# Kernel optimization log

Hardware: AMD Instinct MI355X
Metric: run time of the kernel (lower is better)

The kernel has to match this reference:

```python
import jax, jax.numpy as jnp
import numpy as np
from jax import lax

B, C, H, W = 16, 128, 128, 128
K = 3
EPS = 1e-8


def setup_inputs() -> dict:
    key = jax.random.key(0)
    k1, k2, k3 = jax.random.split(key, 3)
    x = jax.random.normal(k1, (B, C, H, W), dtype=jnp.float32)
    style = jax.random.normal(k2, (B, C), dtype=jnp.float32)
    weight = jax.random.normal(k3, (C, C, K, K), dtype=jnp.float32)
    return {"x": x, "style": style, "weight": weight}


def reference(x, style, weight):
    b = x.shape[0]
    o, i, kh, kw = weight.shape
    h, w_sp = x.shape[2], x.shape[3]
    # style / ||style||_inf over channel dim (per-sample scalar)
    s = style / jnp.max(jnp.abs(style), axis=1, keepdims=True)          # (B, i)
    # weight * (1/sqrt(i*kh*kw)) / ||weight||_inf over (i,kh,kw) per out channel
    wmax = jnp.max(jnp.abs(weight), axis=(1, 2, 3), keepdims=True)      # (o,1,1,1)
    wn = weight * (1.0 / jnp.sqrt(jnp.float32(i * kh * kw)) / wmax)     # (o,i,kh,kw)
    # per-sample modulation over input channels
    wmod = wn[None] * s[:, None, :, None, None]                         # (B,o,i,kh,kw)
    # demodulation (coe reshaped to (i,1,1,1) in torch; valid since o==i)
    coe = lax.rsqrt(jnp.sum(jnp.square(wmod), axis=(2, 3, 4)) + EPS)    # (B,o)
    wmod = wmod * coe[:, :, None, None, None]
    # fused batched conv via grouped-conv trick (StyleGAN2-style)
    xr = x.reshape(1, b * i, h, w_sp)
    wr = wmod.reshape(b * o, i, kh, kw)
    out = lax.conv_general_dilated(
        xr, wr,
        window_strides=(1, 1),
        padding=[(1, 1), (1, 1)],
        feature_group_count=b,
        dimension_numbers=("NCHW", "OIHW", "NCHW"),
    )
    return out.reshape(b, o, h, w_sp)
```

## Files before the change

### kernel.cpp

```cpp
#include <hip/hip_runtime.h>
#include <hip/hip_bf16.h>


#define BATCH 16
#define CH    128
#define HW    128
#define WPITCH 1152

#define WS_WMAX 0
#define WS_SN   128
#define WS_AFAC 2176
#define WS_WT   4224
#define WFRAG_BYTE_OFF 606720
#define WFRAG_BYTES    4718592
#define WS_NEEDED      (WFRAG_BYTE_OFF + WFRAG_BYTES)

typedef short  s8v  __attribute__((ext_vector_type(8)));
typedef float  f4v  __attribute__((ext_vector_type(4)));
typedef float  f2v  __attribute__((ext_vector_type(2)));

__device__ inline unsigned short f2bf(float f) {
    union { float f; unsigned int u; } v; v.f = f;
    unsigned int r = v.u + 0x7FFFu + ((v.u >> 16) & 1u);
    return (unsigned short)(r >> 16);
}

__global__ __launch_bounds__(256) void k0_transpose(const float* __restrict__ w,
                                                    float* __restrict__ ws) {
    int idx = blockIdx.x * 256 + threadIdx.x;
    if (idx < CH * WPITCH) {
        int kt = idx >> 7;
        int o  = idx & 127;
        ws[WS_WT + idx] = w[(size_t)o * WPITCH + kt];
    }
}

__global__ __launch_bounds__(256) void k1_norms(const float* __restrict__ style,
                                                const float* __restrict__ weight,
                                                float* __restrict__ ws) {
    __shared__ float red[4];
    const int bid = blockIdx.x;
    const int t = threadIdx.x;
    if (bid < 128) {
        const int o = bid;
        float m = 0.f;
        for (int idx = t; idx < WPITCH; idx += 256)
            m = fmaxf(m, fabsf(weight[(size_t)o * WPITCH + idx]));
        #pragma unroll
        for (int off = 32; off > 0; off >>= 1)
            m = fmaxf(m, __shfl_down(m, off, 64));
        if ((t & 63) == 0) red[t >> 6] = m;
        __syncthreads();
        if (t == 0)
            ws[WS_WMAX + o] = fmaxf(fmaxf(red[0], red[1]), fmaxf(red[2], red[3]));
    } else {
        const int b = bid - 128;
        float v = (t < CH) ? style[b * CH + t] : 0.f;
        float m = fabsf(v);
        #pragma unroll
        for (int off = 32; off > 0; off >>= 1)
            m = fmaxf(m, __shfl_down(m, off, 64));
        if ((t & 63) == 0) red[t >> 6] = m;
        __syncthreads();
        float smax = fmaxf(fmaxf(red[0], red[1]), fmaxf(red[2], red[3]));
        if (t < CH) ws[WS_SN + b * CH + t] = v / smax;
    }
}

__global__ __launch_bounds__(256) void k2_coe(const float* __restrict__ weight,
                                              float* __restrict__ ws) {
    const int o = blockIdx.x;
    const int b = blockIdx.y;
    const int t = threadIdx.x;
    const float* sn = ws + WS_SN + b * CH;
    float s = 0.f;
    for (int idx = t; idx < WPITCH; idx += 256) {
        int i = idx / 9;
        float v = weight[(size_t)o * WPITCH + idx] * sn[i];
        s += v * v;
    }
    #pragma unroll
    for (int off = 32; off > 0; off >>= 1) s += __shfl_down(s, off, 64);
    __shared__ float red[4];
    if ((t & 63) == 0) red[t >> 6] = s;
    __syncthreads();
    if (t == 0) {
        float S = red[0] + red[1] + red[2] + red[3];
        float wm = ws[WS_WMAX + o];
        float scale = 1.0f / (sqrtf(1152.0f) * wm);
        float coe = rsqrtf(scale * scale * S + 1e-8f);
        ws[WS_AFAC + b * CH + o] = scale * coe;
    }
}

__global__ __launch_bounds__(256) void k3_swz(const float* __restrict__ ws,
                                              const float* __restrict__ weight,
                                              unsigned short* __restrict__ wfrag) {
    int t = blockIdx.x * 256 + threadIdx.x;
    const int lane = t & 63;
    int f = t >> 6;
    const int mo = f & 7;  f >>= 3;
    const int ci = f & 3;  f >>= 2;
    const int kk = f % 9;
    const int b  = f / 9;
    const int o  = mo * 16 + (lane & 15);
    const int i0 = ci * 32 + (lane >> 4) * 8;
    const float af = ws[WS_AFAC + b * CH + o];
    union { unsigned short u[8]; uint4 v; } pk;
    #pragma unroll
    for (int j = 0; j < 8; ++j) {
        int i = i0 + j;
        float v = weight[(size_t)o * WPITCH + i * 9 + kk] * af * ws[WS_SN + b * CH + i];
        pk.u[j] = f2bf(v);
    }
    *(uint4*)(wfrag + (size_t)t * 8) = pk.v;
}

#define XROW 132
#define XIP  40

__global__ __launch_bounds__(256, 2) void k4_mfma(const float* __restrict__ x,
                                                  const unsigned short* __restrict__ wfrag,
                                                  float* __restrict__ out) {
    const int h0 = blockIdx.x * 2;
    const int b  = blockIdx.y;
    const int t  = threadIdx.x;
    const int lane = t & 63;
    const int w    = t >> 6;
    const int ohalf = w & 1;
    const int rsel  = w >> 1;
    const int ln15  = lane & 15;
    const int quad  = lane >> 4;

    __shared__ unsigned short xT[4 * XROW * XIP];

    if (t < 32) {
        const int zr   = t & 3;
        const int zibk = (t >> 2) & 3;
        const int zc   = (t >> 4) ? 129 : 0;
        *(s8v*)&xT[(zr * XROW + zc) * XIP + zibk * 8] = (s8v){0, 0, 0, 0, 0, 0, 0, 0};
    }

    f4v acc[4][8];
    #pragma unroll
    for (int mt = 0; mt < 4; ++mt)
        #pragma unroll
        for (int nt = 0; nt < 8; ++nt)
            acc[mt][nt] = (f4v){0.f, 0.f, 0.f, 0.f};

    const int  cp     = t & 63;
    const int  sr     = w;
    const int  srow   = h0 - 1 + sr;
    const bool svalid = (unsigned)srow < 128u;
    const int  srcl   = svalid ? srow : 0;

    #pragma unroll 1
    for (int ci = 0; ci < 4; ++ci) {
        const int ib = ci * 32;
        __syncthreads();

        #pragma unroll
        for (int it = 0; it < 4; ++it) {
            const float* xp = x + (((size_t)(b * CH + ib + it * 8)) * HW + srcl) * HW + 2 * cp;
            f2v d[8];
            #pragma unroll
            for (int j = 0; j < 8; ++j)
                d[j] = *(const f2v*)(xp + (size_t)j * HW * HW);
            union { unsigned short u[16]; s8v v[2]; } pk;
            #pragma unroll
            for (int j = 0; j < 8; ++j) {
                pk.u[j]     = f2bf(svalid ? d[j].x : 0.f);
                pk.u[8 + j] = f2bf(svalid ? d[j].y : 0.f);
            }
            *(s8v*)&xT[(sr * XROW + (2 * cp + 1)) * XIP + it * 8] = pk.v[0];
            *(s8v*)&xT[(sr * XROW + (2 * cp + 2)) * XIP + it * 8] = pk.v[1];
        }
        __syncthreads();

        s8v aN[4];
        #pragma unroll
        for (int mt = 0; mt < 4; ++mt) {
            const int mo = ohalf * 4 + mt;
            aN[mt] = *(const s8v*)(wfrag +
                     ((size_t)(((b * 9 + 0) * 4 + ci) * 8 + mo) * 64 + lane) * 8);
        }
        #pragma unroll 1
        for (int kk = 0; kk < 9; ++kk) {
            s8v aC[4];
            #pragma unroll
            for (int mt = 0; mt < 4; ++mt) aC[mt] = aN[mt];
            const int kn = (kk < 8) ? kk + 1 : 8;
            #pragma unroll
            for (int mt = 0; mt < 4; ++mt) {
                const int mo = ohalf * 4 + mt;
                aN[mt] = *(const s8v*)(wfrag +
                         ((size_t)(((b * 9 + kn) * 4 + ci) * 8 + mo) * 64 + lane) * 8);
            }
            const int ky = kk / 3;
            const int kx = kk - ky * 3;
            const int r  = rsel + ky;
            s8v bf[8];
            #pragma unroll
            for (int nt = 0; nt < 8; ++nt) {
                const int c = nt * 16 + ln15 + kx;
                bf[nt] = *(const s8v*)&xT[(r * XROW + c) * XIP + quad * 8];
            }
            #pragma unroll
            for (int mt = 0; mt < 4; ++mt)
                #pragma unroll
                for (int nt = 0; nt < 8; ++nt)
                    acc[mt][nt] = __builtin_amdgcn_mfma_f32_16x16x32_bf16(
                        aC[mt], bf[nt], acc[mt][nt], 0, 0, 0);
        }
    }

    const int orow = h0 + rsel;
    #pragma unroll
    for (int mt = 0; mt < 4; ++mt) {
        int o = ohalf * 64 + mt * 16 + quad * 4;
        #pragma unroll
        for (int nt = 0; nt < 8; ++nt) {
            int xcol = nt * 16 + ln15;
            float* op = out + (((size_t)(b * CH + o)) * HW + orow) * HW + xcol;
            #pragma unroll
            for (int reg = 0; reg < 4; ++reg)
                op[(size_t)reg * HW * HW] = acc[mt][nt][reg];
        }
    }
}

#define TI    8
#define XPITCH 132
__global__ __launch_bounds__(256) void k3_conv(const float* __restrict__ x,
                                               const float* __restrict__ ws,
                                               float* __restrict__ out) {
    const int h = blockIdx.x;
    const int b = blockIdx.y;
    const int t = threadIdx.x;
    const int og = t >> 4;
    const int pg = t & 15;

    __shared__ float x_lds[TI * 3 * XPITCH];
    __shared__ float w_lds[TI * 9 * 128];
    __shared__ float Af_l[128];
    __shared__ float sn_l[128];

    if (t < 128) {
        Af_l[t] = ws[WS_AFAC + b * CH + t];
        sn_l[t] = ws[WS_SN + b * CH + t];
    }
    float acc[8][8];
    #pragma unroll
    for (int j = 0; j < 8; ++j)
        #pragma unroll
        for (int p = 0; p < 8; ++p) acc[j][p] = 0.f;

    const float4* wt4 = (const float4*)(ws + WS_WT);
    float4* w_lds4 = (float4*)w_lds;
    const float4* Af4 = (const float4*)Af_l;

    #pragma unroll 1
    for (int ci = 0; ci < CH / TI; ++ci) {
        const int ib = ci * TI;
        __syncthreads();
        for (int idx = t; idx < TI * 3 * 130; idx += 256) {
            int ti  = idx / 390;
            int rem = idx - ti * 390;
            int r   = rem / 130;
            int c   = rem - r * 130;
            int row = h + r - 1;
            int col = c - 1;
            float v = 0.f;
            if ((unsigned)row < 128u && (unsigned)col < 128u)
                v = x[(((size_t)b * CH + ib + ti) * HW + row) * HW + col];
            x_lds[(ti * 3 + r) * XPITCH + c] = v;
        }
        for (int idx = t; idx < TI * 9 * 32; idx += 256) {
            int kt = idx >> 5;
            int o4 = idx & 31;
            int ti = kt / 9;
            float4 wv = wt4[(size_t)ib * 9 * 32 + idx];
            float4 af = Af4[o4];
            float  s  = sn_l[ib + ti];
            float4 rr;
            rr.x = wv.x * af.x * s; rr.y = wv.y * af.y * s;
            rr.z = wv.z * af.z * s; rr.w = wv.w * af.w * s;
            w_lds4[idx] = rr;
        }
        __syncthreads();
        #pragma unroll 1
        for (int ti = 0; ti < TI; ++ti) {
            float xv[3][12];
            #pragma unroll
            for (int ky = 0; ky < 3; ++ky)
                #pragma unroll
                for (int q = 0; q < 3; ++q) {
                    float4 v = *(const float4*)&x_lds[(ti * 3 + ky) * XPITCH + pg * 8 + q * 4];
                    xv[ky][q*4+0] = v.x; xv[ky][q*4+1] = v.y;
                    xv[ky][q*4+2] = v.z; xv[ky][q*4+3] = v.w;
                }
            #pragma unroll
            for (int kk = 0; kk < 9; ++kk) {
                const int ky = kk / 3;
                const int kx = kk % 3;
                float wv[8];
                #pragma unroll
                for (int q = 0; q < 2; ++q) {
                    float4 v = *(const float4*)&w_lds[(ti * 9 + kk) * 128 + og * 8 + q * 4];
                    wv[q*4+0] = v.x; wv[q*4+1] = v.y; wv[q*4+2] = v.z; wv[q*4+3] = v.w;
                }
                #pragma unroll
                for (int j = 0; j < 8; ++j)
                    #pragma unroll
                    for (int p = 0; p < 8; ++p)
                        acc[j][p] = fmaf(wv[j], xv[ky][p + kx], acc[j][p]);
            }
        }
    }
    const size_t obase = ((size_t)b * CH) * (HW * HW) + (size_t)h * HW;
    #pragma unroll
    for (int j = 0; j < 8; ++j) {
        int o = og * 8 + j;
        float4 v0 = {acc[j][0], acc[j][1], acc[j][2], acc[j][3]};
        float4 v1 = {acc[j][4], acc[j][5], acc[j][6], acc[j][7]};
        *(float4*)&out[obase + (size_t)o * (HW * HW) + pg * 8]     = v0;
        *(float4*)&out[obase + (size_t)o * (HW * HW) + pg * 8 + 4] = v1;
    }
}

extern "C" void kernel_launch(void* const* d_in, const int* in_sizes, int n_in,
                              void* d_out, int out_size, void* d_ws, size_t ws_size,
                              hipStream_t stream) {
    const float* x      = (const float*)d_in[0];
    const float* style  = (const float*)d_in[1];
    const float* weight = (const float*)d_in[2];
    float* out = (float*)d_out;
    float* ws  = (float*)d_ws;

    k1_norms<<<144, 256, 0, stream>>>(style, weight, ws);
    k2_coe<<<dim3(CH, BATCH), 256, 0, stream>>>(weight, ws);

    if (ws_size >= (size_t)WS_NEEDED) {
        unsigned short* wfrag = (unsigned short*)((char*)d_ws + WFRAG_BYTE_OFF);
        k3_swz<<<1152, 256, 0, stream>>>(ws, weight, wfrag);
        k4_mfma<<<dim3(HW / 2, BATCH), 256, 0, stream>>>(x, wfrag, out);
    } else {
        k0_transpose<<<(CH * WPITCH + 255) / 256, 256, 0, stream>>>(weight, ws);
        k3_conv<<<dim3(HW, BATCH), 256, 0, stream>>>(x, ws, out);
    }
}
```

Before: 313.2 us.

## Fuse weight prep into one kernel and double-buffer x tiles in MFMA conv

Three prep kernels (norms, demod coefficients, fragment swizzle) are merged into a single kprep kernel that stages 16 weight rows in shared memory and writes bf16 MFMA fragments directly, removing two launches and redundant global traffic. The conv kernel now double-buffers the input-channel tile in LDS: loads for the next 32-channel chunk are issued and committed while MFMAs on the current chunk run, with an XOR swizzle on the LDS layout to reduce bank conflicts. The block index is remapped through an XCD-style swizzle and the kk loop is fully unrolled. Costs include double LDS usage, more registers for prefetched data, and a more complex schedule.

```diff
diff --git a/kernel.cpp b/kernel.cpp
--- a/kernel.cpp
+++ b/kernel.cpp
@@ -23,6 +23,222 @@
     union { float f; unsigned int u; } v; v.f = f;
     unsigned int r = v.u + 0x7FFFu + ((v.u >> 16) & 1u);
     return (unsigned short)(r >> 16);
+}
+
+__global__ __launch_bounds__(256) void kprep(const float* __restrict__ style,
+                                             const float* __restrict__ weight,
+                                             unsigned short* __restrict__ wfrag) {
+    const int b  = blockIdx.x >> 3;
+    const int mo = blockIdx.x & 7;
+    const int t  = threadIdx.x;
+
+    __shared__ float wrow[16 * 1153];
+    __shared__ float snl[128];
+    __shared__ float afl[16];
+    __shared__ float red[4];
+
+    float sv = (t < 128) ? style[b * CH + t] : 0.f;
+    float m = fabsf(sv);
+    #pragma unroll
+    for (int off = 32; off > 0; off >>= 1)
+        m = fmaxf(m, __shfl_down(m, off, 64));
+    if ((t & 63) == 0) red[t >> 6] = m;
+
+    for (int idx = t; idx < 16 * 1152; idx += 256) {
+        int r = idx / 1152;
+        int c = idx - r * 1152;
+        wrow[r * 1153 + c] = weight[(size_t)(mo * 16 + r) * WPITCH + c];
+    }
+    __syncthreads();
+    float smax = fmaxf(fmaxf(red[0], red[1]), fmaxf(red[2], red[3]));
+    if (t < 128) snl[t] = sv / smax;
+    __syncthreads();
+
+    const int o16 = t >> 4;
+    const int s   = t & 15;
+    float mx = 0.f, ss = 0.f;
+    for (int c = s; c < 1152; c += 16) {
+        float v = wrow[o16 * 1153 + c];
+        mx = fmaxf(mx, fabsf(v));
+        float u = v * snl[c / 9];
+        ss += u * u;
+    }
+    #pragma unroll
+    for (int off = 8; off > 0; off >>= 1) {
+        mx = fmaxf(mx, __shfl_down(mx, off, 16));
+        ss += __shfl_down(ss, off, 16);
+    }
+    if (s == 0) {
+        float scale = 1.0f / (sqrtf(1152.0f) * mx);
+        afl[o16] = scale * rsqrtf(scale * scale * ss + 1e-8f);
+    }
+    __syncthreads();
+
+    for (int fid = t; fid < 2304; fid += 256) {
+        const int lane = fid & 63;
+        int f2 = fid >> 6;
+        const int ci = f2 & 3;
+        const int kk = f2 >> 2;
+        const int ro = lane & 15;
+        const int i0 = ci * 32 + (lane >> 4) * 8;
+        const float af = afl[ro];
+        union { unsigned short u[8]; uint4 v; } pk;
+        #pragma unroll
+        for (int j = 0; j < 8; ++j) {
+            int i = i0 + j;
+            float v = wrow[ro * 1153 + i * 9 + kk] * af * snl[i];
+            pk.u[j] = f2bf(v);
+        }
+        *(uint4*)(wfrag + ((size_t)(((b * 9 + kk) * 4 + ci) * 8 + mo) * 64 + lane) * 8) = pk.v;
+    }
+}
+
+#define XBUF 16640
+
+__device__ inline int xoff(int r, int c, int qs) { return (r * 130 + c) * 32 + qs * 8; }
+
+__device__ inline const s8v* afrag_ptr(const unsigned short* wfrag, int b, int kk,
+                                       int ci, int mo, int lane) {
+    return (const s8v*)(wfrag + ((size_t)(((b * 9 + kk) * 4 + ci) * 8 + mo) * 64 + lane) * 8);
+}
+
+__global__ __launch_bounds__(256, 2) void k4_mfma(const float* __restrict__ x,
+                                                  const unsigned short* __restrict__ wfrag,
+                                                  float* __restrict__ out) {
+    const int wg  = blockIdx.x;
+    const int swz = (wg & 7) * 128 + (wg >> 3);
+    const int b   = swz >> 6;
+    const int h0  = (swz & 63) * 2;
+
+    const int t    = threadIdx.x;
+    const int lane = t & 63;
+    const int w    = t >> 6;
+    const int ohalf = w & 1;
+    const int rsel  = w >> 1;
+    const int ln15  = lane & 15;
+    const int quad  = lane >> 4;
+
+    __shared__ unsigned short xls[2 * XBUF];
+
+    if (t < 64) {
+        const int zb = (t >> 5) & 1;
+        const int zr = (t >> 3) & 3;
+        const int zc = ((t >> 2) & 1) ? 129 : 0;
+        const int zq = t & 3;
+        *(s8v*)&xls[zb * XBUF + xoff(zr, zc, zq)] = (s8v){0, 0, 0, 0, 0, 0, 0, 0};
+    }
+
+    f4v acc[4][8];
+    #pragma unroll
+    for (int mt = 0; mt < 4; ++mt)
+        #pragma unroll
+        for (int nt = 0; nt < 8; ++nt)
+            acc[mt][nt] = (f4v){0.f, 0.f, 0.f, 0.f};
+
+    const int  cp     = t & 63;
+    const int  sr     = w;
+    const int  srow   = h0 - 1 + sr;
+    const bool svalid = (unsigned)srow < 128u;
+    const int  srcl   = svalid ? srow : 0;
+
+    #pragma unroll
+    for (int it = 0; it < 4; ++it) {
+        const float* xp = x + (((size_t)(b * CH + it * 8)) * HW + srcl) * HW + 2 * cp;
+        union { unsigned short u[16]; s8v v[2]; } pk;
+        #pragma unroll
+        for (int j = 0; j < 8; ++j) {
+            f2v d = *(const f2v*)(xp + (size_t)j * HW * HW);
+            pk.u[j]     = f2bf(svalid ? d.x : 0.f);
+            pk.u[8 + j] = f2bf(svalid ? d.y : 0.f);
+        }
+        *(s8v*)&xls[xoff(sr, 2 * cp + 1, it ^ (cp & 3))]       = pk.v[0];
+        *(s8v*)&xls[xoff(sr, 2 * cp + 2, it ^ ((cp + 1) & 3))] = pk.v[1];
+    }
+    __syncthreads();
+
+#define ISSUE(IT) do { \
+    const float* xp_ = x + (((size_t)(b * CH + ibn + (IT) * 8)) * HW + srcl) * HW + 2 * cp; \
+    _Pragma("unroll") \
+    for (int j = 0; j < 8; ++j) pf[j] = *(const f2v*)(xp_ + (size_t)j * HW * HW); \
+} while (0)
+
+#define COMMIT(IT) do { \
+    union { unsigned short u[16]; s8v v[2]; } pk_; \
+    _Pragma("unroll") \
+    for (int j = 0; j < 8; ++j) { \
+        pk_.u[j]     = f2bf(svalid ? pf[j].x : 0.f); \
+        pk_.u[8 + j] = f2bf(svalid ? pf[j].y : 0.f); } \
+    *(s8v*)&bufn[xoff(sr, 2 * cp + 1, (IT) ^ (cp & 3))]       = pk_.v[0]; \
+    *(s8v*)&bufn[xoff(sr, 2 * cp + 2, (IT) ^ ((cp + 1) & 3))] = pk_.v[1]; \
+} while (0)
+
+    s8v aN[4];
+    #pragma unroll
+    for (int mt = 0; mt < 4; ++mt)
+        aN[mt] = *afrag_ptr(wfrag, b, 0, 0, ohalf * 4 + mt, lane);
+
+    #pragma unroll 1
+    for (int ci = 0; ci < 4; ++ci) {
+        unsigned short* bufc = xls + (ci & 1) * XBUF;
+        unsigned short* bufn = xls + ((ci & 1) ^ 1) * XBUF;
+        const int ibn = (ci + 1) * 32;
+        f2v pf[8];
+
+        #pragma unroll
+        for (int kk = 0; kk < 9; ++kk) {
+            s8v aC[4];
+            #pragma unroll
+            for (int mt = 0; mt < 4; ++mt) aC[mt] = aN[mt];
+            {
+                const int pci = (kk < 8) ? ci : ci + 1;
+                const int pkk = (kk < 8) ? kk + 1 : 0;
+                if (pci < 4) {
+                    #pragma unroll
+                    for (int mt = 0; mt < 4; ++mt)
+                        aN[mt] = *afrag_ptr(wfrag, b, pkk, pci, ohalf * 4 + mt, lane);
+                }
+            }
+            if (ci < 3) {
+                if      (kk == 0) { ISSUE(0); }
+                else if (kk == 2) { COMMIT(0); ISSUE(1); }
+                else if (kk == 4) { COMMIT(1); ISSUE(2); }
+                else if (kk == 6) { COMMIT(2); ISSUE(3); }
+                else if (kk == 8) { COMMIT(3); }
+            }
+            const int ky = kk / 3;
+            const int kx = kk - ky * 3;
+            const int r  = rsel + ky;
+            s8v bf[8];
+            #pragma unroll
+            for (int nt = 0; nt < 8; ++nt) {
+                const int c = nt * 16 + ln15 + kx;
+                bf[nt] = *(const s8v*)&bufc[xoff(r, c, quad ^ ((c >> 1) & 3))];
+            }
+            #pragma unroll
+            for (int mt = 0; mt < 4; ++mt)
+                #pragma unroll
+                for (int nt = 0; nt < 8; ++nt)
+                    acc[mt][nt] = __builtin_amdgcn_mfma_f32_16x16x32_bf16(
+                        aC[mt], bf[nt], acc[mt][nt], 0, 0, 0);
+        }
+        __syncthreads();
+    }
+#undef ISSUE
+#undef COMMIT
+
+    const int orow = h0 + rsel;
+    #pragma unroll
+    for (int mt = 0; mt < 4; ++mt) {
+        int o = ohalf * 64 + mt * 16 + quad * 4;
+        #pragma unroll
+        for (int nt = 0; nt < 8; ++nt) {
+            int xcol = nt * 16 + ln15;
+            float* op = out + (((size_t)(b * CH + o)) * HW + orow) * HW + xcol;
+            #pragma unroll
+            for (int reg = 0; reg < 4; ++reg)
+                op[(size_t)reg * HW * HW] = acc[mt][nt][reg];
+        }
+    }
 }
 
 __global__ __launch_bounds__(256) void k0_transpose(const float* __restrict__ w,
@@ -90,142 +306,6 @@
         float scale = 1.0f / (sqrtf(1152.0f) * wm);
         float coe = rsqrtf(scale * scale * S + 1e-8f);
         ws[WS_AFAC + b * CH + o] = scale * coe;
-    }
-}
-
-__global__ __launch_bounds__(256) void k3_swz(const float* __restrict__ ws,
-                                              const float* __restrict__ weight,
-                                              unsigned short* __restrict__ wfrag) {
-    int t = blockIdx.x * 256 + threadIdx.x;
-    const int lane = t & 63;
-    int f = t >> 6;
-    const int mo = f & 7;  f >>= 3;
-    const int ci = f & 3;  f >>= 2;
-    const int kk = f % 9;
-    const int b  = f / 9;
-    const int o  = mo * 16 + (lane & 15);
-    const int i0 = ci * 32 + (lane >> 4) * 8;
-    const float af = ws[WS_AFAC + b * CH + o];
-    union { unsigned short u[8]; uint4 v; } pk;
-    #pragma unroll
-    for (int j = 0; j < 8; ++j) {
-        int i = i0 + j;
-        float v = weight[(size_t)o * WPITCH + i * 9 + kk] * af * ws[WS_SN + b * CH + i];
-        pk.u[j] = f2bf(v);
-    }
-    *(uint4*)(wfrag + (size_t)t * 8) = pk.v;
-}
-
-#define XROW 132
-#define XIP  40
-
-__global__ __launch_bounds__(256, 2) void k4_mfma(const float* __restrict__ x,
-                                                  const unsigned short* __restrict__ wfrag,
-                                                  float* __restrict__ out) {
-    const int h0 = blockIdx.x * 2;
-    const int b  = blockIdx.y;
-    const int t  = threadIdx.x;
-    const int lane = t & 63;
-    const int w    = t >> 6;
-    const int ohalf = w & 1;
-    const int rsel  = w >> 1;
-    const int ln15  = lane & 15;
-    const int quad  = lane >> 4;
-
-    __shared__ unsigned short xT[4 * XROW * XIP];
-
-    if (t < 32) {
-        const int zr   = t & 3;
-        const int zibk = (t >> 2) & 3;
-        const int zc   = (t >> 4) ? 129 : 0;
-        *(s8v*)&xT[(zr * XROW + zc) * XIP + zibk * 8] = (s8v){0, 0, 0, 0, 0, 0, 0, 0};
-    }
-
-    f4v acc[4][8];
-    #pragma unroll
-    for (int mt = 0; mt < 4; ++mt)
-        #pragma unroll
-        for (int nt = 0; nt < 8; ++nt)
-            acc[mt][nt] = (f4v){0.f, 0.f, 0.f, 0.f};
-
-    const int  cp     = t & 63;
-    const int  sr     = w;
-    const int  srow   = h0 - 1 + sr;
-    const bool svalid = (unsigned)srow < 128u;
-    const int  srcl   = svalid ? srow : 0;
-
-    #pragma unroll 1
-    for (int ci = 0; ci < 4; ++ci) {
-        const int ib = ci * 32;
-        __syncthreads();
-
-        #pragma unroll
-        for (int it = 0; it < 4; ++it) {
-            const float* xp = x + (((size_t)(b * CH + ib + it * 8)) * HW + srcl) * HW + 2 * cp;
-            f2v d[8];
-            #pragma unroll
-            for (int j = 0; j < 8; ++j)
-                d[j] = *(const f2v*)(xp + (size_t)j * HW * HW);
-            union { unsigned short u[16]; s8v v[2]; } pk;
-            #pragma unroll
-            for (int j = 0; j < 8; ++j) {
-                pk.u[j]     = f2bf(svalid ? d[j].x : 0.f);
-                pk.u[8 + j] = f2bf(svalid ? d[j].y : 0.f);
-            }
-            *(s8v*)&xT[(sr * XROW + (2 * cp + 1)) * XIP + it * 8] = pk.v[0];
-            *(s8v*)&xT[(sr * XROW + (2 * cp + 2)) * XIP + it * 8] = pk.v[1];
-        }
-        __syncthreads();
-
-        s8v aN[4];
-        #pragma unroll
-        for (int mt = 0; mt < 4; ++mt) {
-            const int mo = ohalf * 4 + mt;
-            aN[mt] = *(const s8v*)(wfrag +
-                     ((size_t)(((b * 9 + 0) * 4 + ci) * 8 + mo) * 64 + lane) * 8);
-        }
-        #pragma unroll 1
-        for (int kk = 0; kk < 9; ++kk) {
-            s8v aC[4];
-            #pragma unroll
-            for (int mt = 0; mt < 4; ++mt) aC[mt] = aN[mt];
-            const int kn = (kk < 8) ? kk + 1 : 8;
-            #pragma unroll
-            for (int mt = 0; mt < 4; ++mt) {
-                const int mo = ohalf * 4 + mt;
-                aN[mt] = *(const s8v*)(wfrag +
-                         ((size_t)(((b * 9 + kn) * 4 + ci) * 8 + mo) * 64 + lane) * 8);
-            }
-            const int ky = kk / 3;
-            const int kx = kk - ky * 3;
-            const int r  = rsel + ky;
-            s8v bf[8];
-            #pragma unroll
-            for (int nt = 0; nt < 8; ++nt) {
-                const int c = nt * 16 + ln15 + kx;
-                bf[nt] = *(const s8v*)&xT[(r * XROW + c) * XIP + quad * 8];
-            }
-            #pragma unroll
-            for (int mt = 0; mt < 4; ++mt)
-                #pragma unroll
-                for (int nt = 0; nt < 8; ++nt)
-                    acc[mt][nt] = __builtin_amdgcn_mfma_f32_16x16x32_bf16(
-                        aC[mt], bf[nt], acc[mt][nt], 0, 0, 0);
-        }
-    }
-
-    const int orow = h0 + rsel;
-    #pragma unroll
-    for (int mt = 0; mt < 4; ++mt) {
-        int o = ohalf * 64 + mt * 16 + quad * 4;
-        #pragma unroll
-        for (int nt = 0; nt < 8; ++nt) {
-            int xcol = nt * 16 + ln15;
-            float* op = out + (((size_t)(b * CH + o)) * HW + orow) * HW + xcol;
-            #pragma unroll
-            for (int reg = 0; reg < 4; ++reg)
-                op[(size_t)reg * HW * HW] = acc[mt][nt][reg];
-        }
     }
 }
 
@@ -337,15 +417,14 @@
     float* out = (float*)d_out;
     float* ws  = (float*)d_ws;
 
-    k1_norms<<<144, 256, 0, stream>>>(style, weight, ws);
-    k2_coe<<<dim3(CH, BATCH), 256, 0, stream>>>(weight, ws);
-
     if (ws_size >= (size_t)WS_NEEDED) {
         unsigned short* wfrag = (unsigned short*)((char*)d_ws + WFRAG_BYTE_OFF);
-        k3_swz<<<1152, 256, 0, stream>>>(ws, weight, wfrag);
-        k4_mfma<<<dim3(HW / 2, BATCH), 256, 0, stream>>>(x, wfrag, out);
+        kprep<<<128, 256, 0, stream>>>(style, weight, wfrag);
+        k4_mfma<<<1024, 256, 0, stream>>>(x, wfrag, out);
     } else {
         k0_transpose<<<(CH * WPITCH + 255) / 256, 256, 0, stream>>>(weight, ws);
+        k1_norms<<<144, 256, 0, stream>>>(style, weight, ws);
+        k2_coe<<<dim3(CH, BATCH), 256, 0, stream>>>(weight, ws);
         k3_conv<<<dim3(HW, BATCH), 256, 0, stream>>>(x, ws, out);
     }
 }
```

Measured after the change: 497.3 us. 1.59x slower.
